# Kernel optimization log

Measured on AMD Instinct MI355X. Metric: run time of the kernel, lower is better.

## Reference

```python
import jax, jax.numpy as jnp
import numpy as np

H, O, L, T, B = 1024, 8192, 2, 64, 256


def setup_inputs() -> dict:
    key = jax.random.key(0)
    ks = jax.random.split(key, 9)
    s = 0.03  # ~1/sqrt(H) scaling to keep tanh out of saturation
    return {
        "x": jax.random.normal(ks[0], (1, B, H), jnp.float32),
        "hidden": jax.random.normal(ks[1], (L, B, H), jnp.float32),
        "embedded": jax.random.normal(ks[2], (T, B, H), jnp.float32),
        "W_ih": jax.random.normal(ks[3], (L, H, H), jnp.float32) * s,
        "W_hh": jax.random.normal(ks[4], (L, H, H), jnp.float32) * s,
        "b_ih": jax.random.normal(ks[5], (L, H), jnp.float32) * s,
        "b_hh": jax.random.normal(ks[6], (L, H), jnp.float32) * s,
        "fc_W": jax.random.normal(ks[7], (O, H), jnp.float32) * s,
        "fc_b": jax.random.normal(ks[8], (O,), jnp.float32) * s,
    }


def reference(x, hidden, embedded, W_ih, W_hh, b_ih, b_hh, fc_W, fc_b):
    # tf_ratio = 0.0 (default): teacher forcing never fires, x <- rnn output.
    # Each torch step runs a 1-step, L-layer tanh RNN then fc; embedded only sets T.
    T_steps = embedded.shape[0]
    x0 = x[0]  # [B, H]

    def rnn_cell(inp, h):  # inp [B,H], h [L,B,H] -> (top_out [B,H], new_h [L,B,H])
        new_h = []
        for l in range(W_ih.shape[0]):  # small fixed layer count
            hl = jnp.tanh(inp @ W_ih[l].T + b_ih[l] + h[l] @ W_hh[l].T + b_hh[l])
            new_h.append(hl)
            inp = hl
        return inp, jnp.stack(new_h, axis=0)

    def body(carry, _):
        xi, h = carry
        out, h = rnn_cell(xi, h)
        logits = out @ fc_W.T + fc_b  # [B, O]
        return (out, h), logits

    (_, _), outs = jax.lax.scan(body, (x0, hidden), None, length=T_steps)
    # torch stacks [1,B,O] slices along dim 0 -> [T,1,B,O]
    return outs[:, None, :, :]
```

## Files before the change

### kernel.cpp

```cpp
#include <hip/hip_runtime.h>
#include <hip/hip_fp16.h>
#include <cmath>

#define HD 1024
#define OD 8192
#define BD 256
#define TD 64

typedef _Float16 h16;
typedef __attribute__((ext_vector_type(8))) _Float16 half8;
typedef __attribute__((ext_vector_type(4))) float floatx4;

__device__ __forceinline__ void async_cp16(const void* g, void* l) {
  __builtin_amdgcn_global_load_lds((const __attribute__((address_space(1))) void*)g,
                                   (__attribute__((address_space(3))) void*)l,
                                   16, 0, 0);
}

#define WAITVM(N) asm volatile("s_waitcnt vmcnt(" #N ")" ::: "memory")

__launch_bounds__(256)
__global__ void gemm_fc(const h16* __restrict__ A, int lda,
                        const h16* __restrict__ B, int ldb,
                        const float* __restrict__ bias, int K,
                        float* __restrict__ out, int ldo) {
  constexpr int BM = 128, BN = 128;
  __shared__ h16 As[BM * 64];
  __shared__ h16 Bs[BN * 64];

  const int tid = threadIdx.x;
  const int lane = tid & 63;
  const int wave = tid >> 6;
  const int wm = wave & 1, wn = wave >> 1;
  const int m0 = blockIdx.y * BM;
  const int n0 = blockIdx.x * BN;

  floatx4 acc[4][4] = {};
  const int fr = lane & 15;
  const int kq = lane >> 4;

  for (int k0 = 0; k0 < K; k0 += 64) {
#pragma unroll
    for (int i = 0; i < 4; ++i) {
      int c = tid + i * 256;
      int row = c >> 3, j8 = c & 7;
      int k8 = j8 ^ (row & 7);
      async_cp16(A + (size_t)(m0 + row) * lda + k0 + k8 * 8, &As[c * 8]);
    }
#pragma unroll
    for (int i = 0; i < 4; ++i) {
      int c = tid + i * 256;
      int row = c >> 3, j8 = c & 7;
      int k8 = j8 ^ (row & 7);
      async_cp16(B + (size_t)(n0 + row) * ldb + k0 + k8 * 8, &Bs[c * 8]);
    }
    __syncthreads();

#pragma unroll
    for (int kk = 0; kk < 2; ++kk) {
      half8 af[4], bf[4];
      int k8g = kk * 4 + kq;
#pragma unroll
      for (int mi = 0; mi < 4; ++mi) {
        int row = wm * 64 + mi * 16 + fr;
        af[mi] = *(const half8*)&As[(row * 8 + (k8g ^ (row & 7))) * 8];
      }
#pragma unroll
      for (int ni = 0; ni < 4; ++ni) {
        int row = wn * 64 + ni * 16 + fr;
        bf[ni] = *(const half8*)&Bs[(row * 8 + (k8g ^ (row & 7))) * 8];
      }
#pragma unroll
      for (int mi = 0; mi < 4; ++mi)
#pragma unroll
        for (int ni = 0; ni < 4; ++ni)
          acc[mi][ni] = __builtin_amdgcn_mfma_f32_16x16x32_f16(af[mi], bf[ni], acc[mi][ni], 0, 0, 0);
    }
    __syncthreads();
  }

#pragma unroll
  for (int mi = 0; mi < 4; ++mi)
#pragma unroll
    for (int ni = 0; ni < 4; ++ni) {
      int colg = n0 + wn * 64 + ni * 16 + fr;
      float bv = bias[colg];
#pragma unroll
      for (int i = 0; i < 4; ++i) {
        int rowg = m0 + wm * 64 + mi * 16 + kq * 4 + i;
        out[(size_t)rowg * ldo + colg] = acc[mi][ni][i] + bv;
      }
    }
}

__launch_bounds__(256)
__global__ void cell_gemm(const h16* __restrict__ A,
                          const h16* __restrict__ Bh, const h16* __restrict__ Bl,
                          const float* __restrict__ bias,
                          h16* __restrict__ d1, int c1,
                          h16* __restrict__ d2, int c2,
                          h16* __restrict__ d3) {
  constexpr int DEPTH = 6;
  __shared__ h16 smem[DEPTH][4][32 * 64];

  const int tid = threadIdx.x;
  const int lane = tid & 63;
  const int wave = tid >> 6;
  const int wm = wave & 1, wn = wave >> 1;
  const int m0 = blockIdx.y * 32;
  const int n0 = blockIdx.x * 32;

  floatx4 acc = {};
  const int fr = lane & 15;
  const int kq = lane >> 4;

  const int c = tid;
  const int row = c >> 3, j8 = c & 7;
  const int k8 = j8 ^ (row & 7);
  const h16* a_hi = A + (size_t)(m0 + row) * 4096 + k8 * 8;
  const h16* a_lo = a_hi + 2048;
  const h16* b_hi = Bh + (size_t)(n0 + row) * 2048 + k8 * 8;
  const h16* b_lo = Bl + (size_t)(n0 + row) * 2048 + k8 * 8;

  auto stage = [&](int buf, int k0) {
    async_cp16(a_hi + k0, &smem[buf][0][c * 8]);
    async_cp16(a_lo + k0, &smem[buf][1][c * 8]);
    async_cp16(b_hi + k0, &smem[buf][2][c * 8]);
    async_cp16(b_lo + k0, &smem[buf][3][c * 8]);
  };

  const int ra = wm * 16 + fr;
  const int rb = wn * 16 + fr;
  auto compute = [&](int buf) {
#pragma unroll
    for (int kk = 0; kk < 2; ++kk) {
      int k8g = kk * 4 + kq;
      int sa = (ra * 8 + (k8g ^ (ra & 7))) * 8;
      int sb = (rb * 8 + (k8g ^ (rb & 7))) * 8;
      half8 ah = *(const half8*)&smem[buf][0][sa];
      half8 al = *(const half8*)&smem[buf][1][sa];
      half8 bh = *(const half8*)&smem[buf][2][sb];
      half8 bl = *(const half8*)&smem[buf][3][sb];
      acc = __builtin_amdgcn_mfma_f32_16x16x32_f16(ah, bh, acc, 0, 0, 0);
      acc = __builtin_amdgcn_mfma_f32_16x16x32_f16(al, bh, acc, 0, 0, 0);
      acc = __builtin_amdgcn_mfma_f32_16x16x32_f16(ah, bl, acc, 0, 0, 0);
    }
  };

#pragma unroll
  for (int s = 0; s < DEPTH; ++s) stage(s, s * 64);

  int buf = 0;
  for (int k = 0; k < 32 - DEPTH; ++k) {
    WAITVM(20);
    __builtin_amdgcn_s_barrier();
    compute(buf);
    __builtin_amdgcn_s_barrier();
    stage(buf, (k + DEPTH) * 64);
    buf = (buf + 1 == DEPTH) ? 0 : buf + 1;
  }
#define CELL_TAIL(N)                 \
  WAITVM(N);                         \
  __builtin_amdgcn_s_barrier();      \
  compute(buf);                      \
  buf = (buf + 1 == DEPTH) ? 0 : buf + 1;
  CELL_TAIL(20)
  CELL_TAIL(16)
  CELL_TAIL(12)
  CELL_TAIL(8)
  CELL_TAIL(4)
  CELL_TAIL(0)
#undef CELL_TAIL

  const int colg = n0 + wn * 16 + fr;
  const float bv = bias[colg];
#pragma unroll
  for (int i = 0; i < 4; ++i) {
    int rowg = m0 + wm * 16 + kq * 4 + i;
    float t = tanhf(acc[i] + bv);
    h16 hi = (h16)t;
    h16 lo = (h16)(t - (float)hi);
    size_t r4 = (size_t)rowg * 4096;
    d1[r4 + c1 + colg] = hi;
    d1[r4 + 2048 + c1 + colg] = lo;
    d2[r4 + c2 + colg] = hi;
    d2[r4 + 2048 + c2 + colg] = lo;
    if (d3) d3[(size_t)rowg * HD + colg] = hi;
  }
}

__global__ void pack_split_w(const float* __restrict__ Wih, const float* __restrict__ Whh,
                             h16* __restrict__ Wh, h16* __restrict__ Wl) {
  int idx = blockIdx.x * 256 + threadIdx.x;
  int n = idx >> 11, k = idx & 2047;
  float v = (k < HD) ? Wih[n * HD + k] : Whh[n * HD + (k - HD)];
  h16 hi = (h16)v;
  Wh[idx] = hi;
  Wl[idx] = (h16)(v - (float)hi);
}

__global__ void cvt_fp16_4(const float* __restrict__ src, h16* __restrict__ dst, int n4) {
  int i = blockIdx.x * 256 + threadIdx.x;
  if (i < n4) {
    float4 v = ((const float4*)src)[i];
    union { h16 h[4]; unsigned long long u; } o;
    o.h[0] = (h16)v.x; o.h[1] = (h16)v.y; o.h[2] = (h16)v.z; o.h[3] = (h16)v.w;
    ((unsigned long long*)dst)[i] = o.u;
  }
}

__global__ void bias_sum(const float* __restrict__ bih, const float* __restrict__ bhh,
                         float* __restrict__ bsum) {
  int i = blockIdx.x * 256 + threadIdx.x;
  bsum[i] = bih[i] + bhh[i];
}

__global__ void init_states(const float* __restrict__ x, const float* __restrict__ hidden,
                            h16* __restrict__ A0, h16* __restrict__ A1) {
  int idx = blockIdx.x * 256 + threadIdx.x;
  if (idx < BD * 2048) {
    int b = idx >> 11, k = idx & 2047;
    float v = (k < HD) ? x[b * HD + k] : hidden[b * HD + (k - HD)];
    h16 hi = (h16)v;
    A0[(size_t)b * 4096 + k] = hi;
    A0[(size_t)b * 4096 + 2048 + k] = (h16)(v - (float)hi);
  } else {
    int r = idx - BD * 2048;
    int b = r >> 10, k = r & 1023;
    float v = hidden[BD * HD + b * HD + k];
    h16 hi = (h16)v;
    A1[(size_t)b * 4096 + 1024 + k] = hi;
    A1[(size_t)b * 4096 + 2048 + 1024 + k] = (h16)(v - (float)hi);
  }
}

extern "C" void kernel_launch(void* const* d_in, const int* in_sizes, int n_in,
                              void* d_out, int out_size, void* d_ws, size_t ws_size,
                              hipStream_t stream) {
  const float* x      = (const float*)d_in[0];
  const float* hidden = (const float*)d_in[1];
  const float* W_ih = (const float*)d_in[3];
  const float* W_hh = (const float*)d_in[4];
  const float* b_ih = (const float*)d_in[5];
  const float* b_hh = (const float*)d_in[6];
  const float* fc_W = (const float*)d_in[7];
  const float* fc_b = (const float*)d_in[8];
  float* out = (float*)d_out;

  char* ws = (char*)d_ws;
  size_t off = 0;
  auto alloc = [&](size_t bytes) {
    void* p = ws + off;
    off += (bytes + 255) & ~(size_t)255;
    return p;
  };
  h16* W0h  = (h16*)alloc((size_t)HD * 2048 * 2);
  h16* W0l  = (h16*)alloc((size_t)HD * 2048 * 2);
  h16* W1h  = (h16*)alloc((size_t)HD * 2048 * 2);
  h16* W1l  = (h16*)alloc((size_t)HD * 2048 * 2);
  h16* fcWh = (h16*)alloc((size_t)OD * HD * 2);
  float* bsum = (float*)alloc(2 * HD * 4);
  h16* A0   = (h16*)alloc(2 * (size_t)BD * 4096 * 2);
  h16* A1   = (h16*)alloc(2 * (size_t)BD * 4096 * 2);
  h16* h1all = (h16*)alloc((size_t)TD * BD * HD * 2);

  pack_split_w<<<8192, 256, 0, stream>>>(W_ih, W_hh, W0h, W0l);
  pack_split_w<<<8192, 256, 0, stream>>>(W_ih + HD * HD, W_hh + HD * HD, W1h, W1l);
  cvt_fp16_4<<<OD * HD / 4 / 256, 256, 0, stream>>>(fc_W, fcWh, OD * HD / 4);
  bias_sum<<<8, 256, 0, stream>>>(b_ih, b_hh, bsum);
  init_states<<<3072, 256, 0, stream>>>(x, hidden, A0, A1);

  dim3 gR(HD / 32, BD / 32);
  for (int t = 0; t < TD; ++t) {
    int p = t & 1, q = p ^ 1;
    h16* A0p = A0 + (size_t)p * BD * 4096;
    h16* A0q = A0 + (size_t)q * BD * 4096;
    h16* A1p = A1 + (size_t)p * BD * 4096;
    h16* A1q = A1 + (size_t)q * BD * 4096;
    cell_gemm<<<gR, 256, 0, stream>>>(A0p, W0h, W0l, bsum,
                                      A1p, 0, A0q + 1024, 0, nullptr);
    cell_gemm<<<gR, 256, 0, stream>>>(A1p, W1h, W1l, bsum + HD,
                                      A0q, 0, A1q + 1024, 0, h1all + (size_t)t * BD * HD);
  }

  dim3 gF(OD / 128, TD * BD / 128);
  gemm_fc<<<gF, 256, 0, stream>>>(h1all, HD, fcWh, HD, fc_b, HD, out, OD);
}
```

Measured before the change: 2.151 ms.

## Split-K the recurrent cell GEMM across two wave groups and double-buffer fc GEMM

The cell GEMM now launches 512 threads per block, and two groups of four waves each handle half of the K dimension. Their partial accumulators are summed through shared memory before the tanh epilogue. This targets latency in the 128 serial cell launches, which each run only 256 blocks. Separately, the final fc GEMM gets a double-buffered async-load pipeline and a launch-bounds occupancy hint, so loads overlap with MFMA work. The cost is extra shared-memory traffic and barriers for the reduction, plus more LDS per block.

```diff
diff --git a/kernel.cpp b/kernel.cpp
--- a/kernel.cpp
+++ b/kernel.cpp
@@ -19,14 +19,14 @@
 
 #define WAITVM(N) asm volatile("s_waitcnt vmcnt(" #N ")" ::: "memory")
 
-__launch_bounds__(256)
+__launch_bounds__(256, 2)
 __global__ void gemm_fc(const h16* __restrict__ A, int lda,
                         const h16* __restrict__ B, int ldb,
                         const float* __restrict__ bias, int K,
                         float* __restrict__ out, int ldo) {
   constexpr int BM = 128, BN = 128;
-  __shared__ h16 As[BM * 64];
-  __shared__ h16 Bs[BN * 64];
+  __shared__ h16 As[2][BM * 64];
+  __shared__ h16 Bs[2][BN * 64];
 
   const int tid = threadIdx.x;
   const int lane = tid & 63;
@@ -39,23 +39,24 @@
   const int fr = lane & 15;
   const int kq = lane >> 4;
 
-  for (int k0 = 0; k0 < K; k0 += 64) {
+  auto stage = [&](int buf, int k0) {
 #pragma unroll
     for (int i = 0; i < 4; ++i) {
       int c = tid + i * 256;
       int row = c >> 3, j8 = c & 7;
       int k8 = j8 ^ (row & 7);
-      async_cp16(A + (size_t)(m0 + row) * lda + k0 + k8 * 8, &As[c * 8]);
+      async_cp16(A + (size_t)(m0 + row) * lda + k0 + k8 * 8, &As[buf][c * 8]);
     }
 #pragma unroll
     for (int i = 0; i < 4; ++i) {
       int c = tid + i * 256;
       int row = c >> 3, j8 = c & 7;
       int k8 = j8 ^ (row & 7);
-      async_cp16(B + (size_t)(n0 + row) * ldb + k0 + k8 * 8, &Bs[c * 8]);
-    }
-    __syncthreads();
-
+      async_cp16(B + (size_t)(n0 + row) * ldb + k0 + k8 * 8, &Bs[buf][c * 8]);
+    }
+  };
+
+  auto compute = [&](int buf) {
 #pragma unroll
     for (int kk = 0; kk < 2; ++kk) {
       half8 af[4], bf[4];
@@ -63,12 +64,12 @@
 #pragma unroll
       for (int mi = 0; mi < 4; ++mi) {
         int row = wm * 64 + mi * 16 + fr;
-        af[mi] = *(const half8*)&As[(row * 8 + (k8g ^ (row & 7))) * 8];
+        af[mi] = *(const half8*)&As[buf][(row * 8 + (k8g ^ (row & 7))) * 8];
       }
 #pragma unroll
       for (int ni = 0; ni < 4; ++ni) {
         int row = wn * 64 + ni * 16 + fr;
-        bf[ni] = *(const half8*)&Bs[(row * 8 + (k8g ^ (row & 7))) * 8];
+        bf[ni] = *(const half8*)&Bs[buf][(row * 8 + (k8g ^ (row & 7))) * 8];
       }
 #pragma unroll
       for (int mi = 0; mi < 4; ++mi)
@@ -76,8 +77,27 @@
         for (int ni = 0; ni < 4; ++ni)
           acc[mi][ni] = __builtin_amdgcn_mfma_f32_16x16x32_f16(af[mi], bf[ni], acc[mi][ni], 0, 0, 0);
     }
-    __syncthreads();
-  }
+  };
+
+  const int steps = K >> 6;
+  stage(0, 0);
+  stage(1, 64);
+  int buf = 0;
+  for (int k = 0; k < steps - 2; ++k) {
+    WAITVM(8);
+    __builtin_amdgcn_s_barrier();
+    compute(buf);
+    __builtin_amdgcn_s_barrier();
+    stage(buf, (k + 2) * 64);
+    buf ^= 1;
+  }
+  WAITVM(8);
+  __builtin_amdgcn_s_barrier();
+  compute(buf);
+  buf ^= 1;
+  WAITVM(0);
+  __builtin_amdgcn_s_barrier();
+  compute(buf);
 
 #pragma unroll
   for (int mi = 0; mi < 4; ++mi)
@@ -93,20 +113,22 @@
     }
 }
 
-__launch_bounds__(256)
+__launch_bounds__(512)
 __global__ void cell_gemm(const h16* __restrict__ A,
                           const h16* __restrict__ Bh, const h16* __restrict__ Bl,
                           const float* __restrict__ bias,
                           h16* __restrict__ d1, int c1,
                           h16* __restrict__ d2, int c2,
                           h16* __restrict__ d3) {
-  constexpr int DEPTH = 6;
-  __shared__ h16 smem[DEPTH][4][32 * 64];
+  constexpr int DEPTH = 4;
+  __shared__ h16 smem[DEPTH][2][4][32 * 64];
 
   const int tid = threadIdx.x;
   const int lane = tid & 63;
   const int wave = tid >> 6;
-  const int wm = wave & 1, wn = wave >> 1;
+  const int kg = wave >> 2;
+  const int wsub = wave & 3;
+  const int wm = wsub & 1, wn = wsub >> 1;
   const int m0 = blockIdx.y * 32;
   const int n0 = blockIdx.x * 32;
 
@@ -114,19 +136,20 @@
   const int fr = lane & 15;
   const int kq = lane >> 4;
 
-  const int c = tid;
-  const int row = c >> 3, j8 = c & 7;
+  const int cc = tid & 255;
+  const int row = cc >> 3, j8 = cc & 7;
   const int k8 = j8 ^ (row & 7);
-  const h16* a_hi = A + (size_t)(m0 + row) * 4096 + k8 * 8;
+  const size_t kbase = (size_t)kg * 1024;
+  const h16* a_hi = A + (size_t)(m0 + row) * 4096 + kbase + k8 * 8;
   const h16* a_lo = a_hi + 2048;
-  const h16* b_hi = Bh + (size_t)(n0 + row) * 2048 + k8 * 8;
-  const h16* b_lo = Bl + (size_t)(n0 + row) * 2048 + k8 * 8;
+  const h16* b_hi = Bh + (size_t)(n0 + row) * 2048 + kbase + k8 * 8;
+  const h16* b_lo = Bl + (size_t)(n0 + row) * 2048 + kbase + k8 * 8;
 
   auto stage = [&](int buf, int k0) {
-    async_cp16(a_hi + k0, &smem[buf][0][c * 8]);
-    async_cp16(a_lo + k0, &smem[buf][1][c * 8]);
-    async_cp16(b_hi + k0, &smem[buf][2][c * 8]);
-    async_cp16(b_lo + k0, &smem[buf][3][c * 8]);
+    async_cp16(a_hi + k0, &smem[buf][kg][0][cc * 8]);
+    async_cp16(a_lo + k0, &smem[buf][kg][1][cc * 8]);
+    async_cp16(b_hi + k0, &smem[buf][kg][2][cc * 8]);
+    async_cp16(b_lo + k0, &smem[buf][kg][3][cc * 8]);
   };
 
   const int ra = wm * 16 + fr;
@@ -137,10 +160,10 @@
       int k8g = kk * 4 + kq;
       int sa = (ra * 8 + (k8g ^ (ra & 7))) * 8;
       int sb = (rb * 8 + (k8g ^ (rb & 7))) * 8;
-      half8 ah = *(const half8*)&smem[buf][0][sa];
-      half8 al = *(const half8*)&smem[buf][1][sa];
-      half8 bh = *(const half8*)&smem[buf][2][sb];
-      half8 bl = *(const half8*)&smem[buf][3][sb];
+      half8 ah = *(const half8*)&smem[buf][kg][0][sa];
+      half8 al = *(const half8*)&smem[buf][kg][1][sa];
+      half8 bh = *(const half8*)&smem[buf][kg][2][sb];
+      half8 bl = *(const half8*)&smem[buf][kg][3][sb];
       acc = __builtin_amdgcn_mfma_f32_16x16x32_f16(ah, bh, acc, 0, 0, 0);
       acc = __builtin_amdgcn_mfma_f32_16x16x32_f16(al, bh, acc, 0, 0, 0);
       acc = __builtin_amdgcn_mfma_f32_16x16x32_f16(ah, bl, acc, 0, 0, 0);
@@ -151,41 +174,49 @@
   for (int s = 0; s < DEPTH; ++s) stage(s, s * 64);
 
   int buf = 0;
-  for (int k = 0; k < 32 - DEPTH; ++k) {
-    WAITVM(20);
+  for (int k = 0; k < 16 - DEPTH; ++k) {
+    WAITVM(12);
     __builtin_amdgcn_s_barrier();
     compute(buf);
     __builtin_amdgcn_s_barrier();
     stage(buf, (k + DEPTH) * 64);
-    buf = (buf + 1 == DEPTH) ? 0 : buf + 1;
+    buf = (buf + 1) & (DEPTH - 1);
   }
 #define CELL_TAIL(N)                 \
   WAITVM(N);                         \
   __builtin_amdgcn_s_barrier();      \
   compute(buf);                      \
-  buf = (buf + 1 == DEPTH) ? 0 : buf + 1;
-  CELL_TAIL(20)
-  CELL_TAIL(16)
+  buf = (buf + 1) & (DEPTH - 1);
   CELL_TAIL(12)
   CELL_TAIL(8)
   CELL_TAIL(4)
   CELL_TAIL(0)
 #undef CELL_TAIL
 
-  const int colg = n0 + wn * 16 + fr;
-  const float bv = bias[colg];
-#pragma unroll
-  for (int i = 0; i < 4; ++i) {
-    int rowg = m0 + wm * 16 + kq * 4 + i;
-    float t = tanhf(acc[i] + bv);
-    h16 hi = (h16)t;
-    h16 lo = (h16)(t - (float)hi);
-    size_t r4 = (size_t)rowg * 4096;
-    d1[r4 + c1 + colg] = hi;
-    d1[r4 + 2048 + c1 + colg] = lo;
-    d2[r4 + c2 + colg] = hi;
-    d2[r4 + 2048 + c2 + colg] = lo;
-    if (d3) d3[(size_t)rowg * HD + colg] = hi;
+  __syncthreads();
+  float* fsm = (float*)&smem[0][0][0][0];
+  if (kg == 1) {
+    *(floatx4*)&fsm[(wsub * 64 + lane) * 4] = acc;
+  }
+  __syncthreads();
+  if (kg == 0) {
+    floatx4 other = *(const floatx4*)&fsm[(wsub * 64 + lane) * 4];
+    acc += other;
+    const int colg = n0 + wn * 16 + fr;
+    const float bv = bias[colg];
+#pragma unroll
+    for (int i = 0; i < 4; ++i) {
+      int rowg = m0 + wm * 16 + kq * 4 + i;
+      float t = tanhf(acc[i] + bv);
+      h16 hi = (h16)t;
+      h16 lo = (h16)(t - (float)hi);
+      size_t r4 = (size_t)rowg * 4096;
+      d1[r4 + c1 + colg] = hi;
+      d1[r4 + 2048 + c1 + colg] = lo;
+      d2[r4 + c2 + colg] = hi;
+      d2[r4 + 2048 + c2 + colg] = lo;
+      if (d3) d3[(size_t)rowg * HD + colg] = hi;
+    }
   }
 }
 
@@ -277,9 +308,9 @@
     h16* A0q = A0 + (size_t)q * BD * 4096;
     h16* A1p = A1 + (size_t)p * BD * 4096;
     h16* A1q = A1 + (size_t)q * BD * 4096;
-    cell_gemm<<<gR, 256, 0, stream>>>(A0p, W0h, W0l, bsum,
+    cell_gemm<<<gR, 512, 0, stream>>>(A0p, W0h, W0l, bsum,
                                       A1p, 0, A0q + 1024, 0, nullptr);
-    cell_gemm<<<gR, 256, 0, stream>>>(A1p, W1h, W1l, bsum + HD,
+    cell_gemm<<<gR, 512, 0, stream>>>(A1p, W1h, W1l, bsum + HD,
                                       A0q, 0, A1q + 1024, 0, h1all + (size_t)t * BD * HD);
   }
 
```

Measured after the change: 2.009 ms. 1.07x faster.
